# Kernel tuning notes

Measured on AMD Instinct MI355X. Metric: run time of the kernel, lower is better.

The kernel has to match this reference:

```python
import jax, jax.numpy as jnp
import numpy as np

GRID_SIZE = 128  # D = H = W
N_POINTS = 8388608


def setup_inputs() -> dict:
    key = jax.random.key(0)
    k_grid, k_coords = jax.random.split(key)
    # occupancy grid buffer: binary {0,1} values as float, shape [D, H, W]
    grid = (jax.random.uniform(k_grid, (GRID_SIZE, GRID_SIZE, GRID_SIZE)) > 0.5).astype(jnp.float32)
    # normalized [-1, 1] query coordinates, layout [..., 3] = (x, y, z)
    coords = jax.random.uniform(k_coords, (N_POINTS, 3), minval=-1.0, maxval=1.0, dtype=jnp.float32)
    return {"grid": grid, "coords": coords}


def _trilinear_sample(grid, coords):
    """torch.nn.functional.grid_sample 5D, mode='bilinear', align_corners=False,
    padding_mode='zeros'. grid: [D,H,W]; coords: [N,3] with (x,y,z) where
    x indexes W, y indexes H, z indexes D. Returns [N]."""
    D, H, W = grid.shape
    x, y, z = coords[:, 0], coords[:, 1], coords[:, 2]
    # unnormalize (align_corners=False): pixel = ((c + 1) * size - 1) / 2
    ix = ((x + 1.0) * W - 1.0) * 0.5
    iy = ((y + 1.0) * H - 1.0) * 0.5
    iz = ((z + 1.0) * D - 1.0) * 0.5

    ix0 = jnp.floor(ix)
    iy0 = jnp.floor(iy)
    iz0 = jnp.floor(iz)
    wx = ix - ix0  # fractional weights
    wy = iy - iy0
    wz = iz - iz0
    ix0 = ix0.astype(jnp.int32)
    iy0 = iy0.astype(jnp.int32)
    iz0 = iz0.astype(jnp.int32)

    def gather(zi, yi, xi):
        # zero padding: out-of-bounds corners contribute 0
        valid = ((zi >= 0) & (zi < D) & (yi >= 0) & (yi < H) & (xi >= 0) & (xi < W))
        zc = jnp.clip(zi, 0, D - 1)
        yc = jnp.clip(yi, 0, H - 1)
        xc = jnp.clip(xi, 0, W - 1)
        return jnp.where(valid, grid[zc, yc, xc], 0.0)

    out = (
        gather(iz0,     iy0,     ix0    ) * (1 - wz) * (1 - wy) * (1 - wx)
        + gather(iz0,     iy0,     ix0 + 1) * (1 - wz) * (1 - wy) * wx
        + gather(iz0,     iy0 + 1, ix0    ) * (1 - wz) * wy       * (1 - wx)
        + gather(iz0,     iy0 + 1, ix0 + 1) * (1 - wz) * wy       * wx
        + gather(iz0 + 1, iy0,     ix0    ) * wz       * (1 - wy) * (1 - wx)
        + gather(iz0 + 1, iy0,     ix0 + 1) * wz       * (1 - wy) * wx
        + gather(iz0 + 1, iy0 + 1, ix0    ) * wz       * wy       * (1 - wx)
        + gather(iz0 + 1, iy0 + 1, ix0 + 1) * wz       * wy       * wx
    )
    return out


def reference(grid, coords):
    flat = coords.reshape(-1, 3)
    return _trilinear_sample(grid, flat)
```

## Files before the change

kernel.cpp:

```cpp
#include <hip/hip_runtime.h>


constexpr int GS  = 128;
constexpr int TD  = GS + 1;
constexpr size_t TBL_SIZE = (size_t)TD * TD * TD;

__global__ __launch_bounds__(256)
void pack_kernel(const float* __restrict__ grid, unsigned char* __restrict__ tbl) {
    int i = blockIdx.x * blockDim.x + threadIdx.x;
    if (i >= (int)TBL_SIZE) return;
    int x = i % TD;
    int t = i / TD;
    int y = t % TD;
    int z = t / TD;
    unsigned byte = 0u;
#pragma unroll
    for (int k = 0; k < 8; ++k) {
        int xi = x - 1 + (k & 1);
        int yi = y - 1 + ((k >> 1) & 1);
        int zi = z - 1 + (k >> 2);
        float g = 0.0f;
        if (((unsigned)xi < (unsigned)GS) &
            ((unsigned)yi < (unsigned)GS) &
            ((unsigned)zi < (unsigned)GS))
            g = grid[(zi * GS + yi) * GS + xi];
        byte |= (g != 0.0f ? 1u : 0u) << k;
    }
    tbl[i] = (unsigned char)byte;
}

__global__ __launch_bounds__(256)
void sample_packed(const unsigned char* __restrict__ tbl,
                   const float* __restrict__ coords,
                   float* __restrict__ out, int nt) {
    int t = blockIdx.x * blockDim.x + threadIdx.x;
    if (t >= nt) return;
    const float4* c4 = (const float4*)coords;
    float4 a = c4[3 * t + 0];
    float4 b = c4[3 * t + 1];
    float4 c = c4[3 * t + 2];
    float xs[4] = {a.x, a.w, b.z, c.y};
    float ys[4] = {a.y, b.x, b.w, c.z};
    float zs[4] = {a.z, b.y, c.x, c.w};
    float4 res;
    float* r = &res.x;
#pragma unroll
    for (int i = 0; i < 4; ++i) {
        float ix = fmaf(xs[i], 64.0f, 63.5f);
        float iy = fmaf(ys[i], 64.0f, 63.5f);
        float iz = fmaf(zs[i], 64.0f, 63.5f);
        float fx = floorf(ix), fy = floorf(iy), fz = floorf(iz);
        float wx = ix - fx, wy = iy - fy, wz = iz - fz;
        int xb = (int)fx + 1, yb = (int)fy + 1, zb = (int)fz + 1;
        xb = min(max(xb, 0), GS); yb = min(max(yb, 0), GS); zb = min(max(zb, 0), GS);
        unsigned byte = (unsigned)tbl[(zb * TD + yb) * TD + xb];
        float v0 = (float)( byte       & 1u);
        float v1 = (float)((byte >> 1) & 1u);
        float v2 = (float)((byte >> 2) & 1u);
        float v3 = (float)((byte >> 3) & 1u);
        float v4 = (float)((byte >> 4) & 1u);
        float v5 = (float)((byte >> 5) & 1u);
        float v6 = (float)((byte >> 6) & 1u);
        float v7 = (float)((byte >> 7) & 1u);
        float c00 = v0 + wx * (v1 - v0);
        float c10 = v2 + wx * (v3 - v2);
        float c01 = v4 + wx * (v5 - v4);
        float c11 = v6 + wx * (v7 - v6);
        float c0  = c00 + wy * (c10 - c00);
        float c1  = c01 + wy * (c11 - c01);
        r[i] = c0 + wz * (c1 - c0);
    }
    ((float4*)out)[t] = res;
}

__global__ __launch_bounds__(256)
void sample_direct(const float* __restrict__ grid,
                   const float* __restrict__ coords,
                   float* __restrict__ out, int nt) {
    int t = blockIdx.x * blockDim.x + threadIdx.x;
    if (t >= nt) return;
    const float4* c4 = (const float4*)coords;
    float4 a = c4[3 * t + 0];
    float4 b = c4[3 * t + 1];
    float4 c = c4[3 * t + 2];
    float xs[4] = {a.x, a.w, b.z, c.y};
    float ys[4] = {a.y, b.x, b.w, c.z};
    float zs[4] = {a.z, b.y, c.x, c.w};
    float4 res;
    float* r = &res.x;
#pragma unroll
    for (int i = 0; i < 4; ++i) {
        float ix = fmaf(xs[i], 64.0f, 63.5f);
        float iy = fmaf(ys[i], 64.0f, 63.5f);
        float iz = fmaf(zs[i], 64.0f, 63.5f);
        float fx = floorf(ix), fy = floorf(iy), fz = floorf(iz);
        float wx = ix - fx, wy = iy - fy, wz = iz - fz;
        int x0 = (int)fx, y0 = (int)fy, z0 = (int)fz;
        float v[8];
#pragma unroll
        for (int k = 0; k < 8; ++k) {
            int xi = x0 + (k & 1);
            int yi = y0 + ((k >> 1) & 1);
            int zi = z0 + (k >> 2);
            bool ok = ((unsigned)xi < (unsigned)GS) &
                      ((unsigned)yi < (unsigned)GS) &
                      ((unsigned)zi < (unsigned)GS);
            int xc = min(max(xi, 0), GS - 1);
            int yc = min(max(yi, 0), GS - 1);
            int zc = min(max(zi, 0), GS - 1);
            v[k] = grid[(zc * GS + yc) * GS + xc] * (ok ? 1.0f : 0.0f);
        }
        float c00 = v[0] + wx * (v[1] - v[0]);
        float c10 = v[2] + wx * (v[3] - v[2]);
        float c01 = v[4] + wx * (v[5] - v[4]);
        float c11 = v[6] + wx * (v[7] - v[6]);
        float c0  = c00 + wy * (c10 - c00);
        float c1  = c01 + wy * (c11 - c01);
        r[i] = c0 + wz * (c1 - c0);
    }
    ((float4*)out)[t] = res;
}

extern "C" void kernel_launch(void* const* d_in, const int* in_sizes, int n_in,
                              void* d_out, int out_size, void* d_ws, size_t ws_size,
                              hipStream_t stream) {
    const float* grid   = (const float*)d_in[0];
    const float* coords = (const float*)d_in[1];
    float* out = (float*)d_out;
    int npts = in_sizes[1] / 3;
    int nt = npts / 4;

    if (ws_size >= TBL_SIZE) {
        unsigned char* tbl = (unsigned char*)d_ws;
        int pack_blocks = (int)((TBL_SIZE + 255) / 256);
        pack_kernel<<<pack_blocks, 256, 0, stream>>>(grid, tbl);
        sample_packed<<<(nt + 255) / 256, 256, 0, stream>>>(tbl, coords, out, nt);
    } else {
        sample_direct<<<(nt + 255) / 256, 256, 0, stream>>>(grid, coords, out, nt);
    }
}
```

Before: 202.7 us.

## Build the corner table from a ballot bitmask and sample eight points per thread

Table construction now runs in two stages. A ballot kernel first packs the float grid into a 64-bit-word bitmask, and the table kernel then reads mask words instead of eight scattered floats per byte. The sampling kernel processes eight points per thread with nontemporal coordinate loads and output stores, and issues all eight table lookups before any interpolation to raise memory-level parallelism. This adds an extra launch and more registers per thread, and it assumes the point count is divisible by eight.

After: 212.2 us. 1.05x slower.

```diff
diff --git a/kernel.cpp b/kernel.cpp
--- a/kernel.cpp
+++ b/kernel.cpp
@@ -1,30 +1,54 @@
 #include <hip/hip_runtime.h>
 
 
+typedef float fx4 __attribute__((ext_vector_type(4)));
+
 constexpr int GS  = 128;
 constexpr int TD  = GS + 1;
-constexpr size_t TBL_SIZE = (size_t)TD * TD * TD;
+constexpr size_t TBL_BYTES  = (size_t)TD * TD * TD;
+constexpr size_t MASK_WORDS = (size_t)GS * GS * GS / 64;
+constexpr size_t WS_NEEDED  = TBL_BYTES + 8 * MASK_WORDS + 64;
 
 __global__ __launch_bounds__(256)
-void pack_kernel(const float* __restrict__ grid, unsigned char* __restrict__ tbl) {
+void bitpack_kernel(const float* __restrict__ grid, unsigned long long* __restrict__ mask) {
+    int gid = blockIdx.x * blockDim.x + threadIdx.x;
+    float v = __builtin_nontemporal_load(&grid[gid]);
+    unsigned long long m = __ballot(v != 0.0f);
+    if ((threadIdx.x & 63) == 0) mask[gid >> 6] = m;
+}
+
+__device__ __forceinline__ unsigned bit_at(unsigned long long lo, unsigned long long hi, int xi) {
+    if ((unsigned)xi >= 128u) return 0u;
+    unsigned long long w = (xi < 64) ? lo : hi;
+    return (unsigned)((w >> (xi & 63)) & 1ull);
+}
+
+__global__ __launch_bounds__(256)
+void table_kernel(const unsigned long long* __restrict__ mask, unsigned char* __restrict__ tbl) {
     int i = blockIdx.x * blockDim.x + threadIdx.x;
-    if (i >= (int)TBL_SIZE) return;
+    if (i >= (int)TBL_BYTES) return;
     int x = i % TD;
     int t = i / TD;
     int y = t % TD;
     int z = t / TD;
+    int x0 = x - 1;
     unsigned byte = 0u;
 #pragma unroll
-    for (int k = 0; k < 8; ++k) {
-        int xi = x - 1 + (k & 1);
-        int yi = y - 1 + ((k >> 1) & 1);
-        int zi = z - 1 + (k >> 2);
-        float g = 0.0f;
-        if (((unsigned)xi < (unsigned)GS) &
-            ((unsigned)yi < (unsigned)GS) &
-            ((unsigned)zi < (unsigned)GS))
-            g = grid[(zi * GS + yi) * GS + xi];
-        byte |= (g != 0.0f ? 1u : 0u) << k;
+    for (int dz = 0; dz < 2; ++dz) {
+#pragma unroll
+        for (int dy = 0; dy < 2; ++dy) {
+            int yi = y - 1 + dy, zi = z - 1 + dz;
+            unsigned long long lo = 0ull, hi = 0ull;
+            if (((unsigned)yi < 128u) & ((unsigned)zi < 128u)) {
+                int r = (zi * 128 + yi) * 2;
+                lo = mask[r];
+                hi = mask[r + 1];
+            }
+            unsigned b0 = bit_at(lo, hi, x0);
+            unsigned b1 = bit_at(lo, hi, x0 + 1);
+            int k = dy * 2 + dz * 4;
+            byte |= (b0 << k) | (b1 << (k + 1));
+        }
     }
     tbl[i] = (unsigned char)byte;
 }
@@ -35,25 +59,33 @@
                    float* __restrict__ out, int nt) {
     int t = blockIdx.x * blockDim.x + threadIdx.x;
     if (t >= nt) return;
-    const float4* c4 = (const float4*)coords;
-    float4 a = c4[3 * t + 0];
-    float4 b = c4[3 * t + 1];
-    float4 c = c4[3 * t + 2];
-    float xs[4] = {a.x, a.w, b.z, c.y};
-    float ys[4] = {a.y, b.x, b.w, c.z};
-    float zs[4] = {a.z, b.y, c.x, c.w};
-    float4 res;
-    float* r = &res.x;
+    const fx4* c4 = (const fx4*)coords;
+    fx4 q[6];
 #pragma unroll
-    for (int i = 0; i < 4; ++i) {
-        float ix = fmaf(xs[i], 64.0f, 63.5f);
-        float iy = fmaf(ys[i], 64.0f, 63.5f);
-        float iz = fmaf(zs[i], 64.0f, 63.5f);
+    for (int j = 0; j < 6; ++j) q[j] = __builtin_nontemporal_load(&c4[6 * t + j]);
+    const float* f = (const float*)q;
+
+    float wxa[8], wya[8], wza[8];
+    int addr[8];
+#pragma unroll
+    for (int i = 0; i < 8; ++i) {
+        float ix = fmaf(f[3 * i + 0], 64.0f, 63.5f);
+        float iy = fmaf(f[3 * i + 1], 64.0f, 63.5f);
+        float iz = fmaf(f[3 * i + 2], 64.0f, 63.5f);
         float fx = floorf(ix), fy = floorf(iy), fz = floorf(iz);
-        float wx = ix - fx, wy = iy - fy, wz = iz - fz;
+        wxa[i] = ix - fx; wya[i] = iy - fy; wza[i] = iz - fz;
         int xb = (int)fx + 1, yb = (int)fy + 1, zb = (int)fz + 1;
         xb = min(max(xb, 0), GS); yb = min(max(yb, 0), GS); zb = min(max(zb, 0), GS);
-        unsigned byte = (unsigned)tbl[(zb * TD + yb) * TD + xb];
+        addr[i] = (zb * TD + yb) * TD + xb;
+    }
+    unsigned bytes[8];
+#pragma unroll
+    for (int i = 0; i < 8; ++i) bytes[i] = (unsigned)tbl[addr[i]];
+    float o[8];
+#pragma unroll
+    for (int i = 0; i < 8; ++i) {
+        unsigned byte = bytes[i];
+        float wx = wxa[i], wy = wya[i], wz = wza[i];
         float v0 = (float)( byte       & 1u);
         float v1 = (float)((byte >> 1) & 1u);
         float v2 = (float)((byte >> 2) & 1u);
@@ -68,9 +100,13 @@
         float c11 = v6 + wx * (v7 - v6);
         float c0  = c00 + wy * (c10 - c00);
         float c1  = c01 + wy * (c11 - c01);
-        r[i] = c0 + wz * (c1 - c0);
+        o[i] = c0 + wz * (c1 - c0);
     }
-    ((float4*)out)[t] = res;
+    fx4* o4 = (fx4*)out;
+    fx4 r0 = {o[0], o[1], o[2], o[3]};
+    fx4 r1 = {o[4], o[5], o[6], o[7]};
+    __builtin_nontemporal_store(r0, &o4[2 * t + 0]);
+    __builtin_nontemporal_store(r1, &o4[2 * t + 1]);
 }
 
 __global__ __launch_bounds__(256)
@@ -128,14 +164,21 @@
     const float* coords = (const float*)d_in[1];
     float* out = (float*)d_out;
     int npts = in_sizes[1] / 3;
-    int nt = npts / 4;
 
-    if (ws_size >= TBL_SIZE) {
+    if (ws_size >= WS_NEEDED) {
         unsigned char* tbl = (unsigned char*)d_ws;
-        int pack_blocks = (int)((TBL_SIZE + 255) / 256);
-        pack_kernel<<<pack_blocks, 256, 0, stream>>>(grid, tbl);
+        size_t mask_off = (TBL_BYTES + 7) & ~(size_t)7;
+        unsigned long long* mask = (unsigned long long*)((char*)d_ws + mask_off);
+
+        int vox = GS * GS * GS;
+        bitpack_kernel<<<vox / 256, 256, 0, stream>>>(grid, mask);
+        int tbl_blocks = (int)((TBL_BYTES + 255) / 256);
+        table_kernel<<<tbl_blocks, 256, 0, stream>>>(mask, tbl);
+
+        int nt = npts / 8;
         sample_packed<<<(nt + 255) / 256, 256, 0, stream>>>(tbl, coords, out, nt);
     } else {
+        int nt = npts / 4;
         sample_direct<<<(nt + 255) / 256, 256, 0, stream>>>(grid, coords, out, nt);
     }
 }
```
